# Kernel optimization log

Hardware: AMD Instinct MI355X
Metric: run time of the kernel (lower is better)

## Reference

```python
import jax, jax.numpy as jnp
import numpy as np

N, M, D_IN, D_OUT = 16384, 8192, 512, 512


def setup_inputs() -> dict:
    key = jax.random.key(0)
    k1, k2, k3, k4, k5, k6 = jax.random.split(key, 6)
    return {
        "node_states": jax.random.normal(k1, (N, D_IN), dtype=jnp.float32),
        "sub_event_states": jax.random.normal(k2, (M, D_IN), dtype=jnp.float32),
        "W1": jax.random.normal(k3, (D_IN, D_OUT), dtype=jnp.float32) * 0.02,
        "W2": jax.random.normal(k4, (D_IN, D_OUT), dtype=jnp.float32) * 0.02,
        "W3": jax.random.normal(k5, (D_OUT, 1), dtype=jnp.float32) * 0.02,
        "b3": jax.random.normal(k6, (1,), dtype=jnp.float32) * 0.02,
    }


def reference(node_states, sub_event_states, W1, W2, W3, b3):
    # Original math: squeeze(Dense3(Dense1(node)[:,None,:] + Dense2(sub)[None,:,:]), 2)
    # Dense3 is linear, so Dense3(a + b) = a@W3 + b@W3 + b3; this computes the
    # identical [N, M] score matrix without the [N, M, D] intermediate.
    s1 = (node_states @ W1) @ W3          # [N, 1]
    s2 = (sub_event_states @ W2) @ W3     # [M, 1]
    return s1 + s2.T + b3                 # [N, M]
```

## Files before the change

kernel.cpp:

```cpp
#include <hip/hip_runtime.h>

#define NN 16384
#define MM 8192
#define DD 512

typedef float floatx4 __attribute__((ext_vector_type(4)));

__global__ void __launch_bounds__(256) gemv_w(const float* __restrict__ W1,
                                              const float* __restrict__ W2,
                                              const float* __restrict__ W3,
                                              float* __restrict__ v) {
    int b = blockIdx.x;
    const float* W = (b < DD) ? W1 : W2;
    int row = (b < DD) ? b : b - DD;
    const float* wr = W + (size_t)row * DD;
    int tid = threadIdx.x;
    float sum = 0.f;
    #pragma unroll
    for (int j = tid; j < DD; j += 256) sum += wr[j] * W3[j];
    #pragma unroll
    for (int off = 32; off > 0; off >>= 1) sum += __shfl_down(sum, off, 64);
    __shared__ float ws[4];
    int lane = tid & 63, w = tid >> 6;
    if (lane == 0) ws[w] = sum;
    __syncthreads();
    if (tid == 0) v[b] = ws[0] + ws[1] + ws[2] + ws[3];
}

__global__ void __launch_bounds__(256) row_dots(const float* __restrict__ node,
                                                const float* __restrict__ sub,
                                                const float* __restrict__ v,
                                                const float* __restrict__ b3,
                                                float* __restrict__ s) {
    int wid = threadIdx.x >> 6;
    int lane = threadIdx.x & 63;
    int row = blockIdx.x * 4 + wid;
    const float* x;
    const float* vv;
    float bias;
    if (row < NN) {
        x = node + (size_t)row * DD;
        vv = v;
        bias = 0.f;
    } else {
        x = sub + (size_t)(row - NN) * DD;
        vv = v + DD;
        bias = b3[0];
    }
    const floatx4* x4 = (const floatx4*)x;
    const floatx4* v4 = (const floatx4*)vv;
    floatx4 a0 = x4[lane],      c0 = v4[lane];
    floatx4 a1 = x4[lane + 64], c1 = v4[lane + 64];
    float sum = a0.x * c0.x + a0.y * c0.y + a0.z * c0.z + a0.w * c0.w
              + a1.x * c1.x + a1.y * c1.y + a1.z * c1.z + a1.w * c1.w;
    #pragma unroll
    for (int off = 32; off > 0; off >>= 1) sum += __shfl_down(sum, off, 64);
    if (lane == 0) s[row] = sum + bias;
}

__global__ void __launch_bounds__(256) add_outer(const float* __restrict__ s1,
                                                 const float* __restrict__ s2,
                                                 floatx4* __restrict__ out) {
    int j4 = blockIdx.x * 256 + threadIdx.x;
    int i0 = blockIdx.y * 32;
    floatx4 b = ((const floatx4*)s2)[j4];
    const float* s1p = s1 + i0;
    floatx4* o = out + (size_t)i0 * (MM / 4) + j4;
    #pragma unroll
    for (int k = 0; k < 32; ++k) {
        float a = s1p[k];
        floatx4 vo;
        vo.x = a + b.x; vo.y = a + b.y; vo.z = a + b.z; vo.w = a + b.w;
        __builtin_nontemporal_store(vo, &o[(size_t)k * (MM / 4)]);
    }
}

extern "C" void kernel_launch(void* const* d_in, const int* in_sizes, int n_in,
                              void* d_out, int out_size, void* d_ws, size_t ws_size,
                              hipStream_t stream) {
    const float* node = (const float*)d_in[0];
    const float* sub  = (const float*)d_in[1];
    const float* W1   = (const float*)d_in[2];
    const float* W2   = (const float*)d_in[3];
    const float* W3   = (const float*)d_in[4];
    const float* b3   = (const float*)d_in[5];
    float* out = (float*)d_out;

    float* ws = (float*)d_ws;
    float* v  = ws;
    float* s  = ws + 1024;

    gemv_w<<<2 * DD, 256, 0, stream>>>(W1, W2, W3, v);

    row_dots<<<(NN + MM) / 4, 256, 0, stream>>>(node, sub, v, b3, s);

    dim3 grid(MM / 4 / 256, NN / 32);
    add_outer<<<grid, 256, 0, stream>>>(s, s + NN, (floatx4*)out);
}
```

Before: 106.7 us.

## Fuse node row-dot computation into outer-sum output kernel

```diff
diff --git a/kernel.cpp b/kernel.cpp
--- a/kernel.cpp
+++ b/kernel.cpp
@@ -27,51 +27,65 @@
     if (tid == 0) v[b] = ws[0] + ws[1] + ws[2] + ws[3];
 }
 
-__global__ void __launch_bounds__(256) row_dots(const float* __restrict__ node,
-                                                const float* __restrict__ sub,
-                                                const float* __restrict__ v,
-                                                const float* __restrict__ b3,
-                                                float* __restrict__ s) {
+__global__ void __launch_bounds__(256) s2_dots(const float* __restrict__ sub,
+                                               const float* __restrict__ v2,
+                                               const float* __restrict__ b3,
+                                               float* __restrict__ s2) {
     int wid = threadIdx.x >> 6;
     int lane = threadIdx.x & 63;
     int row = blockIdx.x * 4 + wid;
-    const float* x;
-    const float* vv;
-    float bias;
-    if (row < NN) {
-        x = node + (size_t)row * DD;
-        vv = v;
-        bias = 0.f;
-    } else {
-        x = sub + (size_t)(row - NN) * DD;
-        vv = v + DD;
-        bias = b3[0];
-    }
-    const floatx4* x4 = (const floatx4*)x;
-    const floatx4* v4 = (const floatx4*)vv;
+    const floatx4* x4 = (const floatx4*)(sub + (size_t)row * DD);
+    const floatx4* v4 = (const floatx4*)v2;
     floatx4 a0 = x4[lane],      c0 = v4[lane];
     floatx4 a1 = x4[lane + 64], c1 = v4[lane + 64];
     float sum = a0.x * c0.x + a0.y * c0.y + a0.z * c0.z + a0.w * c0.w
               + a1.x * c1.x + a1.y * c1.y + a1.z * c1.z + a1.w * c1.w;
     #pragma unroll
     for (int off = 32; off > 0; off >>= 1) sum += __shfl_down(sum, off, 64);
-    if (lane == 0) s[row] = sum + bias;
+    if (lane == 0) s2[row] = sum + b3[0];
 }
 
-__global__ void __launch_bounds__(256) add_outer(const float* __restrict__ s1,
-                                                 const float* __restrict__ s2,
-                                                 floatx4* __restrict__ out) {
-    int j4 = blockIdx.x * 256 + threadIdx.x;
-    int i0 = blockIdx.y * 32;
-    floatx4 b = ((const floatx4*)s2)[j4];
-    const float* s1p = s1 + i0;
-    floatx4* o = out + (size_t)i0 * (MM / 4) + j4;
+__global__ void __launch_bounds__(256) fused_rows(const float* __restrict__ node,
+                                                  const float* __restrict__ v1,
+                                                  const float* __restrict__ s2,
+                                                  floatx4* __restrict__ out) {
+    __shared__ float s1s[16];
+    int tid = threadIdx.x;
+    int wid = tid >> 6, lane = tid & 63;
+    int i0 = blockIdx.x * 16;
+
+    const floatx4* v4 = (const floatx4*)v1;
+    floatx4 c0 = v4[lane], c1 = v4[lane + 64];
     #pragma unroll
-    for (int k = 0; k < 32; ++k) {
-        float a = s1p[k];
-        floatx4 vo;
-        vo.x = a + b.x; vo.y = a + b.y; vo.z = a + b.z; vo.w = a + b.w;
-        __builtin_nontemporal_store(vo, &o[(size_t)k * (MM / 4)]);
+    for (int r = 0; r < 4; ++r) {
+        int row = i0 + wid * 4 + r;
+        const floatx4* x4 = (const floatx4*)(node + (size_t)row * DD);
+        floatx4 a0 = x4[lane], a1 = x4[lane + 64];
+        float sum = a0.x * c0.x + a0.y * c0.y + a0.z * c0.z + a0.w * c0.w
+                  + a1.x * c1.x + a1.y * c1.y + a1.z * c1.z + a1.w * c1.w;
+        #pragma unroll
+        for (int off = 32; off > 0; off >>= 1) sum += __shfl_down(sum, off, 64);
+        if (lane == 0) s1s[wid * 4 + r] = sum;
+    }
+    __syncthreads();
+
+    floatx4 b[8];
+    const floatx4* s2v = (const floatx4*)s2;
+    #pragma unroll
+    for (int c = 0; c < 8; ++c) b[c] = s2v[tid + 256 * c];
+
+    floatx4* obase = out + (size_t)i0 * (MM / 4) + tid;
+    #pragma unroll 4
+    for (int k = 0; k < 16; ++k) {
+        float a = s1s[k];
+        floatx4* orow = obase + (size_t)k * (MM / 4);
+        #pragma unroll
+        for (int c = 0; c < 8; ++c) {
+            floatx4 vo;
+            vo.x = a + b[c].x; vo.y = a + b[c].y;
+            vo.z = a + b[c].z; vo.w = a + b[c].w;
+            __builtin_nontemporal_store(vo, &orow[256 * c]);
+        }
     }
 }
 
@@ -88,12 +102,11 @@
 
     float* ws = (float*)d_ws;
     float* v  = ws;
-    float* s  = ws + 1024;
+    float* s2 = ws + 1024;
 
     gemv_w<<<2 * DD, 256, 0, stream>>>(W1, W2, W3, v);
 
-    row_dots<<<(NN + MM) / 4, 256, 0, stream>>>(node, sub, v, b3, s);
+    s2_dots<<<MM / 4, 256, 0, stream>>>(sub, v + DD, b3, s2);
 
-    dim3 grid(MM / 4 / 256, NN / 32);
-    add_outer<<<grid, 256, 0, stream>>>(s, s + NN, (floatx4*)out);
+    fused_rows<<<NN / 16, 256, 0, stream>>>(node, v, s2, (floatx4*)out);
 }
```

Result: slower. 118.5 us (+11.2%).
